# Kernel optimization log

Measured on AMD Instinct MI355X. Metric: run time of the kernel, lower is better.

The kernel has to match this reference:

```python
import jax, jax.numpy as jnp
import numpy as np

B, C, T = 128, 9, 2048
R = T // 4            # reduced_timesteps after two MaxPool1d(2)
N = B * R             # total graph nodes
E_SINGLE = 8192       # edges per sample graph (avg degree 16 over R nodes)
HID = 128
OUT = 12


def setup_inputs():
    key = jax.random.key(0)
    ks = jax.random.split(key, 14)
    x = jax.random.normal(ks[0], (B, C, T), jnp.float32)
    # per-sample graph, replicated with offset i*R per batch element (as in forward)
    single = jax.random.randint(ks[1], (2, E_SINGLE), 0, R)
    offsets = (jnp.arange(B) * R)[None, :, None]
    edge_index = (single[:, None, :] + offsets).reshape(2, -1)  # [2, B*E_SINGLE]

    def lin(k, fan_in, shape):
        return jax.random.normal(k, shape, jnp.float32) / np.sqrt(fan_in)

    return {
        "x": x,
        "edge_index": edge_index,
        "conv1_w": lin(ks[2], C * 5, (16, C, 5)),
        "conv1_b": jnp.zeros((16,), jnp.float32),
        "conv2_w": lin(ks[3], 16 * 5, (32, 16, 5)),
        "conv2_b": jnp.zeros((32,), jnp.float32),
        "gcn1_w": lin(ks[4], 32, (32, HID)),
        "gcn1_b": jnp.zeros((HID,), jnp.float32),
        "gcn2_w": lin(ks[5], HID, (HID, HID)),
        "gcn2_b": jnp.zeros((HID,), jnp.float32),
        "fc_w": lin(ks[6], HID, (HID, OUT)),
        "fc_b": jnp.zeros((OUT,), jnp.float32),
    }


def _gcn_conv(h, edge_index, w, b, n):
    # PyG GCNConv: linear -> add self-loops -> sym-normalized sum aggregation -> + bias
    h = h @ w
    loops = jnp.arange(n)
    row = jnp.concatenate([edge_index[0], loops])  # source
    col = jnp.concatenate([edge_index[1], loops])  # target (aggregation)
    deg = jax.ops.segment_sum(jnp.ones(col.shape, h.dtype), col, num_segments=n)
    dis = jnp.where(deg > 0, jax.lax.rsqrt(jnp.maximum(deg, 1e-12)), 0.0)
    norm = dis[row] * dis[col]                      # [E+N]
    out = jax.ops.segment_sum(norm[:, None] * h[row], col, num_segments=n)
    return out + b


def _temporal_conv(x, w1, b1, w2, b2):
    dn = ("NCH", "OIH", "NCH")
    h = jax.lax.conv_general_dilated(x, w1, (1,), [(2, 2)], dimension_numbers=dn)
    h = jax.nn.relu(h + b1[None, :, None])
    h = jax.lax.reduce_window(h, -jnp.inf, jax.lax.max, (1, 1, 2), (1, 1, 2), "VALID")
    h = jax.lax.conv_general_dilated(h, w2, (1,), [(2, 2)], dimension_numbers=dn)
    h = jax.nn.relu(h + b2[None, :, None])
    h = jax.lax.reduce_window(h, -jnp.inf, jax.lax.max, (1, 1, 2), (1, 1, 2), "VALID")
    return h  # [B, 32, R]


def reference(x, edge_index, conv1_w, conv1_b, conv2_w, conv2_b,
              gcn1_w, gcn1_b, gcn2_w, gcn2_b, fc_w, fc_b):
    h = _temporal_conv(x, conv1_w, conv1_b, conv2_w, conv2_b)   # [B, 32, R]
    nodes = h.transpose(0, 2, 1).reshape(B * R, 32)             # [N, 32]
    g = jax.nn.relu(_gcn_conv(nodes, edge_index, gcn1_w, gcn1_b, N))
    g = jax.nn.relu(_gcn_conv(g, edge_index, gcn2_w, gcn2_b, N))
    g = g.reshape(B, R, HID).mean(axis=1)                       # [B, HID]
    return g @ fc_w + fc_b                                      # [B, OUT]
```

## Files before the change

kernel.cpp:

```cpp
#include <hip/hip_runtime.h>
#include <hip/hip_bf16.h>

#define BB   128
#define CIN  9
#define TT   2048
#define RR   512
#define NN   (BB*RR)
#define HID  128
#define NOUT 12

typedef __attribute__((ext_vector_type(8))) short short8;
typedef __attribute__((ext_vector_type(4))) float f32x4;

static __device__ inline unsigned short f2bf(float f) {
    unsigned int u = __float_as_uint(f);
    unsigned int r = (u + 0x7fffu + ((u >> 16) & 1u)) >> 16;
    return (unsigned short)r;
}
static __device__ inline float bf2f(unsigned short u) {
    return __uint_as_float(((unsigned int)u) << 16);
}

__global__ __launch_bounds__(256) void k_prep(const int* __restrict__ ei, int E, int es,
        float* __restrict__ Af32, float* __restrict__ dis,
        const float* __restrict__ g2w, unsigned short* __restrict__ w2t) {
    int tid = threadIdx.x;
    if (blockIdx.x == 0) {
        __shared__ int cnt[512];
        cnt[tid] = 0; cnt[tid + 256] = 0;
        __syncthreads();
        for (int i = tid; i < es; i += 256) atomicAdd(&cnt[ei[E + i]], 1);
        __syncthreads();
        dis[tid]       = rsqrtf((float)cnt[tid] + 1.0f);
        dis[tid + 256] = rsqrtf((float)cnt[tid + 256] + 1.0f);
        for (int idx = tid; idx < 128 * 128; idx += 256) {
            int c2 = idx >> 7, f = idx & 127;
            w2t[f * 128 + c2] = f2bf(g2w[idx]);
        }
    } else {
        float4* dst = (float4*)(Af32 + (size_t)(blockIdx.x - 1) * 2048);
        float4 z = make_float4(0.f, 0.f, 0.f, 0.f);
        dst[tid] = z;
        dst[tid + 256] = z;
    }
}

__global__ __launch_bounds__(256) void k_scatter(const int* __restrict__ ei, int E, int es,
        const float* __restrict__ dis, float* __restrict__ Af32) {
    int i = blockIdx.x * 256 + threadIdx.x;
    if (i < es) {
        int row = ei[i], col = ei[E + i];
        atomicAdd(&Af32[col * 512 + row], dis[row] * dis[col]);
    } else if (i < es + 512) {
        int r = i - es;
        float d = dis[r];
        atomicAdd(&Af32[r * 512 + r], d * d);
    }
}

__global__ __launch_bounds__(512) void k_convs(const float* __restrict__ x,
        const float* __restrict__ w1, const float* __restrict__ b1,
        const float* __restrict__ w2, const float* __restrict__ b2,
        unsigned short* __restrict__ nodesT,
        const float* __restrict__ Af32, unsigned short* __restrict__ Ab16) {
    __shared__ float sx[CIN][268];
    __shared__ float s1[16][132];
    int tid = threadIdx.x;

    if (blockIdx.x >= 1024) {
        int idx0 = (((blockIdx.x - 1024) << 9) + tid) << 3;
        float4 v0 = *(const float4*)&Af32[idx0];
        float4 v1 = *(const float4*)&Af32[idx0 + 4];
        ushort4 o0, o1;
        o0.x = f2bf(v0.x); o0.y = f2bf(v0.y); o0.z = f2bf(v0.z); o0.w = f2bf(v0.w);
        o1.x = f2bf(v1.x); o1.y = f2bf(v1.y); o1.z = f2bf(v1.z); o1.w = f2bf(v1.w);
        *(ushort4*)&Ab16[idx0] = o0;
        *(ushort4*)&Ab16[idx0 + 4] = o1;
        return;
    }

    int cb = blockIdx.x;
    int b  = cb >> 3;
    int r0 = (cb & 7) * 64;
    int wv   = __builtin_amdgcn_readfirstlane(tid >> 6);
    int lane = tid & 63;

    for (int idx = tid; idx < CIN * 268; idx += 512) {
        int c = idx / 268, j = idx - c * 268;
        int g = 4 * r0 - 6 + j;
        float v = 0.f;
        if (g >= 0 && g < TT) v = x[(b * CIN + c) * TT + g];
        sx[c][j] = v;
    }
    __syncthreads();

    {
        int c1a = wv * 2, c1b = wv * 2 + 1;
        float biasA = b1[c1a], biasB = b1[c1b];
        for (int pp = lane; pp < 132; pp += 64) {
            int p = 2 * r0 - 2 + pp;
            float valA = 0.f, valB = 0.f;
            if (p >= 0 && p < 1024) {
                float a0A = biasA, a1A = biasA, a0B = biasB, a1B = biasB;
#pragma unroll
                for (int c = 0; c < CIN; ++c) {
                    const float2* px = (const float2*)&sx[c][2 * pp];
                    float2 q0 = px[0], q1 = px[1], q2 = px[2];
                    {
                        const float* wp = &w1[(c1a * CIN + c) * 5];
                        float k0 = wp[0], k1 = wp[1], k2 = wp[2], k3 = wp[3], k4 = wp[4];
                        a0A += q0.x*k0 + q0.y*k1 + q1.x*k2 + q1.y*k3 + q2.x*k4;
                        a1A += q0.y*k0 + q1.x*k1 + q1.y*k2 + q2.x*k3 + q2.y*k4;
                    }
                    {
                        const float* wp = &w1[(c1b * CIN + c) * 5];
                        float k0 = wp[0], k1 = wp[1], k2 = wp[2], k3 = wp[3], k4 = wp[4];
                        a0B += q0.x*k0 + q0.y*k1 + q1.x*k2 + q1.y*k3 + q2.x*k4;
                        a1B += q0.y*k0 + q1.x*k1 + q1.y*k2 + q2.x*k3 + q2.y*k4;
                    }
                }
                valA = fmaxf(fmaxf(a0A, a1A), 0.f);
                valB = fmaxf(fmaxf(a0B, a1B), 0.f);
            }
            s1[c1a][pp] = valA;
            s1[c1b][pp] = valB;
        }
    }
    __syncthreads();

    int rl = lane;
    float acc0[4], acc1[4];
#pragma unroll
    for (int o = 0; o < 4; ++o) {
        float bv = b2[wv * 4 + o];
        acc0[o] = bv; acc1[o] = bv;
    }
#pragma unroll
    for (int c = 0; c < 16; ++c) {
        const float2* ps = (const float2*)&s1[c][2 * rl];
        float2 q0 = ps[0], q1 = ps[1], q2 = ps[2];
#pragma unroll
        for (int o = 0; o < 4; ++o) {
            const float* wp = &w2[((wv * 4 + o) * 16 + c) * 5];
            float k0 = wp[0], k1 = wp[1], k2 = wp[2], k3 = wp[3], k4 = wp[4];
            acc0[o] += q0.x*k0 + q0.y*k1 + q1.x*k2 + q1.y*k3 + q2.x*k4;
            acc1[o] += q0.y*k0 + q1.x*k1 + q1.y*k2 + q2.x*k3 + q2.y*k4;
        }
    }
    int n = r0 + rl;
    unsigned short* np = nodesT + ((size_t)b * 32 + wv * 4) * 512 + n;
    np[0]    = f2bf(fmaxf(fmaxf(acc0[0], acc1[0]), 0.f));
    np[512]  = f2bf(fmaxf(fmaxf(acc0[1], acc1[1]), 0.f));
    np[1024] = f2bf(fmaxf(fmaxf(acc0[2], acc1[2]), 0.f));
    np[1536] = f2bf(fmaxf(fmaxf(acc0[3], acc1[3]), 0.f));
}

__global__ __launch_bounds__(256) void k_agg1(const unsigned short* __restrict__ Ab,
        const unsigned short* __restrict__ nT, const float* __restrict__ w1,
        const float* __restrict__ b1, unsigned short* __restrict__ h16) {
    __shared__ unsigned short sA[128][72];
    __shared__ unsigned short sN[32][72];
    __shared__ float sAgg[128][33];
    __shared__ float sw1[32 * 128];
    int tid = threadIdx.x;
    int b  = blockIdx.x >> 2;
    int rb = blockIdx.x & 3;
    int r0 = rb * 128;
    const unsigned short* nb = nT + (size_t)b * 32 * 512;

    {
        const float4* src = (const float4*)w1;
        float4* dst = (float4*)sw1;
#pragma unroll
        for (int i = 0; i < 4; ++i) dst[tid + i * 256] = src[tid + i * 256];
    }

    int wv = tid >> 6, lane = tid & 63;
    int l15 = lane & 15, quad = lane >> 4;
    int mB = wv * 32;
    f32x4 acc[2][2];
#pragma unroll
    for (int i = 0; i < 2; ++i)
#pragma unroll
        for (int j = 0; j < 2; ++j) acc[i][j] = (f32x4){0.f, 0.f, 0.f, 0.f};

    for (int kt = 0; kt < 8; ++kt) {
        int k0 = kt * 64;
        __syncthreads();
#pragma unroll
        for (int i = 0; i < 8; ++i) {
            int idx = tid + i * 256;
            int row = idx >> 4, c4 = (idx & 15) * 4;
            *(ushort4*)&sA[row][c4] = *(const ushort4*)&Ab[(size_t)(r0 + row) * 512 + k0 + c4];
        }
#pragma unroll
        for (int i = 0; i < 2; ++i) {
            int idx = tid + i * 256;
            int f = idx >> 4, c4 = (idx & 15) * 4;
            *(ushort4*)&sN[f][c4] = *(const ushort4*)&nb[(size_t)f * 512 + k0 + c4];
        }
        __syncthreads();
#pragma unroll
        for (int ks = 0; ks < 2; ++ks) {
            int kk = ks * 32 + quad * 8;
            short8 av0 = *(const short8*)&sA[mB + l15][kk];
            short8 av1 = *(const short8*)&sA[mB + 16 + l15][kk];
            short8 bv0 = *(const short8*)&sN[l15][kk];
            short8 bv1 = *(const short8*)&sN[16 + l15][kk];
            acc[0][0] = __builtin_amdgcn_mfma_f32_16x16x32_bf16(av0, bv0, acc[0][0], 0, 0, 0);
            acc[0][1] = __builtin_amdgcn_mfma_f32_16x16x32_bf16(av0, bv1, acc[0][1], 0, 0, 0);
            acc[1][0] = __builtin_amdgcn_mfma_f32_16x16x32_bf16(av1, bv0, acc[1][0], 0, 0, 0);
            acc[1][1] = __builtin_amdgcn_mfma_f32_16x16x32_bf16(av1, bv1, acc[1][1], 0, 0, 0);
        }
    }
    __syncthreads();
#pragma unroll
    for (int mi = 0; mi < 2; ++mi)
#pragma unroll
        for (int ni = 0; ni < 2; ++ni)
#pragma unroll
            for (int r = 0; r < 4; ++r)
                sAgg[mB + mi * 16 + quad * 4 + r][ni * 16 + l15] = acc[mi][ni][r];
    __syncthreads();

    int fq = tid & 31;
    int ng = tid >> 5;
    float4 bv = *(const float4*)&b1[fq * 4];
    for (int ch = 0; ch < 4; ++ch) {
        float a[4][4];
#pragma unroll
        for (int j = 0; j < 4; ++j)
#pragma unroll
            for (int q = 0; q < 4; ++q) a[j][q] = 0.f;
#pragma unroll
        for (int c = 0; c < 32; ++c) {
            float4 wvv = *(const float4*)&sw1[c * 128 + fq * 4];
#pragma unroll
            for (int j = 0; j < 4; ++j) {
                float xc = sAgg[ch * 32 + ng * 4 + j][c];
                a[j][0] += xc * wvv.x; a[j][1] += xc * wvv.y;
                a[j][2] += xc * wvv.z; a[j][3] += xc * wvv.w;
            }
        }
#pragma unroll
        for (int j = 0; j < 4; ++j) {
            ushort4 o;
            o.x = f2bf(fmaxf(a[j][0] + bv.x, 0.f));
            o.y = f2bf(fmaxf(a[j][1] + bv.y, 0.f));
            o.z = f2bf(fmaxf(a[j][2] + bv.z, 0.f));
            o.w = f2bf(fmaxf(a[j][3] + bv.w, 0.f));
            *(ushort4*)&h16[(size_t)(b * 512 + r0 + ch * 32 + ng * 4 + j) * 128 + fq * 4] = o;
        }
    }
}

__global__ __launch_bounds__(256) void k_lin2(const unsigned short* __restrict__ g16,
        const unsigned short* __restrict__ w2t, unsigned short* __restrict__ tT) {
    __shared__ __align__(16) unsigned short smem2[64 * 136 + 128 * 136];
    unsigned short (*srow)[136] = (unsigned short (*)[136])smem2;
    unsigned short (*swT)[136]  = (unsigned short (*)[136])&smem2[64 * 136];
    unsigned short (*sOut)[72]  = (unsigned short (*)[72])smem2;
    int tid = threadIdx.x;
    int nbase = blockIdx.x * 64;

    {
        const ushort4* src = (const ushort4*)(g16 + (size_t)nbase * 128);
#pragma unroll
        for (int i = 0; i < 8; ++i) {
            int idx = tid + i * 256;
            int row = idx >> 5, col4 = idx & 31;
            ushort4 v = src[idx];
            *(ushort4*)&srow[row][col4 * 4] = v;
        }
    }
    {
        const ushort4* src = (const ushort4*)w2t;
#pragma unroll
        for (int i = 0; i < 16; ++i) {
            int idx = tid + i * 256;
            int f = idx >> 5, c4 = idx & 31;
            ushort4 v = src[idx];
            *(ushort4*)&swT[f][c4 * 4] = v;
        }
    }
    __syncthreads();

    int wv  = tid >> 6;
    int lane = tid & 63;
    int m0 = wv * 16;
    int l15 = lane & 15;
    int quad = lane >> 4;
    f32x4 acc[8];
#pragma unroll
    for (int nt = 0; nt < 8; ++nt) acc[nt] = (f32x4){0.f, 0.f, 0.f, 0.f};
#pragma unroll
    for (int kc = 0; kc < 4; ++kc) {
        int k0 = kc * 32 + quad * 8;
        short8 a = *(const short8*)&srow[m0 + l15][k0];
#pragma unroll
        for (int nt = 0; nt < 8; ++nt) {
            short8 b = *(const short8*)&swT[nt * 16 + l15][k0];
            acc[nt] = __builtin_amdgcn_mfma_f32_16x16x32_bf16(a, b, acc[nt], 0, 0, 0);
        }
    }
    __syncthreads();

#pragma unroll
    for (int nt = 0; nt < 8; ++nt) {
        ushort4 o;
        o.x = f2bf(acc[nt][0]); o.y = f2bf(acc[nt][1]);
        o.z = f2bf(acc[nt][2]); o.w = f2bf(acc[nt][3]);
        *(ushort4*)&sOut[nt * 16 + l15][m0 + quad * 4] = o;
    }
    __syncthreads();

    int b = nbase >> 9;
    int rl0 = nbase & 511;
#pragma unroll
    for (int i = 0; i < 8; ++i) {
        int idx = tid + i * 256;
        int col = idx >> 4, r4 = (idx & 15) * 4;
        ushort4 v = *(ushort4*)&sOut[col][r4];
        *(ushort4*)&tT[((size_t)(b * 128 + col)) * 512 + rl0 + r4] = v;
    }
}

__global__ __launch_bounds__(256) void k_agg2(const unsigned short* __restrict__ Ab,
        const unsigned short* __restrict__ tT, const float* __restrict__ b2,
        float* __restrict__ partial) {
    __shared__ unsigned short sA[128][72];
    __shared__ unsigned short sB[128][72];
    __shared__ float sred[2][128];
    int tid = threadIdx.x;
    int b  = blockIdx.x >> 2;
    int rb = blockIdx.x & 3;
    int r0 = rb * 128;
    const unsigned short* tb = tT + (size_t)b * 128 * 512;
    int wv = tid >> 6, lane = tid & 63;
    int l15 = lane & 15, quad = lane >> 4;
    int wr = wv >> 1, wc = wv & 1;
    f32x4 acc[4][4];
#pragma unroll
    for (int i = 0; i < 4; ++i)
#pragma unroll
        for (int j = 0; j < 4; ++j) acc[i][j] = (f32x4){0.f, 0.f, 0.f, 0.f};

    for (int kt = 0; kt < 8; ++kt) {
        int k0 = kt * 64;
        __syncthreads();
#pragma unroll
        for (int i = 0; i < 8; ++i) {
            int idx = tid + i * 256;
            int row = idx >> 4, c4 = (idx & 15) * 4;
            *(ushort4*)&sA[row][c4] = *(const ushort4*)&Ab[(size_t)(r0 + row) * 512 + k0 + c4];
        }
#pragma unroll
        for (int i = 0; i < 8; ++i) {
            int idx = tid + i * 256;
            int row = idx >> 4, c4 = (idx & 15) * 4;
            *(ushort4*)&sB[row][c4] = *(const ushort4*)&tb[(size_t)row * 512 + k0 + c4];
        }
        __syncthreads();
#pragma unroll
        for (int ks = 0; ks < 2; ++ks) {
            int kk = ks * 32 + quad * 8;
            short8 av[4], bfr[4];
#pragma unroll
            for (int mi = 0; mi < 4; ++mi)
                av[mi] = *(const short8*)&sA[wr * 64 + mi * 16 + l15][kk];
#pragma unroll
            for (int ni = 0; ni < 4; ++ni)
                bfr[ni] = *(const short8*)&sB[wc * 64 + ni * 16 + l15][kk];
#pragma unroll
            for (int mi = 0; mi < 4; ++mi)
#pragma unroll
                for (int ni = 0; ni < 4; ++ni)
                    acc[mi][ni] = __builtin_amdgcn_mfma_f32_16x16x32_bf16(av[mi], bfr[ni], acc[mi][ni], 0, 0, 0);
        }
    }

#pragma unroll
    for (int ni = 0; ni < 4; ++ni) {
        int col = wc * 64 + ni * 16 + l15;
        float bc = b2[col];
        float s = 0.f;
#pragma unroll
        for (int mi = 0; mi < 4; ++mi)
#pragma unroll
            for (int r = 0; r < 4; ++r)
                s += fmaxf(acc[mi][ni][r] + bc, 0.f);
        s += __shfl_xor(s, 16);
        s += __shfl_xor(s, 32);
        if (quad == 0) sred[wr][col] = s;
    }
    __syncthreads();
    if (tid < 128)
        partial[(size_t)blockIdx.x * 128 + tid] = sred[0][tid] + sred[1][tid];
}

__global__ __launch_bounds__(128) void k_fc(const float* __restrict__ partial,
        const float* __restrict__ fw, const float* __restrict__ fb,
        float* __restrict__ out) {
    __shared__ float sm[HID];
    int b = blockIdx.x, f = threadIdx.x;
    float acc = 0.f;
#pragma unroll
    for (int j = 0; j < 4; ++j) acc += partial[(size_t)(b * 4 + j) * 128 + f];
    sm[f] = acc * (1.0f / RR);
    __syncthreads();
    if (f < NOUT) {
        float s = fb[f];
#pragma unroll
        for (int c = 0; c < HID; ++c) s += sm[c] * fw[c * NOUT + f];
        out[b * NOUT + f] = s;
    }
}

extern "C" void kernel_launch(void* const* d_in, const int* in_sizes, int n_in,
                              void* d_out, int out_size, void* d_ws, size_t ws_size,
                              hipStream_t stream) {
    const float* x   = (const float*)d_in[0];
    const int*   ei  = (const int*)d_in[1];
    const float* c1w = (const float*)d_in[2];
    const float* c1b = (const float*)d_in[3];
    const float* c2w = (const float*)d_in[4];
    const float* c2b = (const float*)d_in[5];
    const float* g1w = (const float*)d_in[6];
    const float* g1b = (const float*)d_in[7];
    const float* g2w = (const float*)d_in[8];
    const float* g2b = (const float*)d_in[9];
    const float* fw  = (const float*)d_in[10];
    const float* fb  = (const float*)d_in[11];
    float* out = (float*)d_out;
    int E  = in_sizes[1] / 2;
    int es = E / BB;

    char* ws = (char*)d_ws;
    unsigned short* nodesT = (unsigned short*)(ws);
    unsigned short* h1     = (unsigned short*)(ws + (4u << 20));
    unsigned short* tT     = (unsigned short*)(ws + (20u << 20));
    float* Af32            = (float*)(ws + (36u << 20));
    unsigned short* Ab16   = (unsigned short*)(ws + (37u << 20));
    float* partial         = (float*)(ws + (37u << 20) + (512u << 10));
    float* dis             = (float*)(ws + (37u << 20) + (768u << 10));
    unsigned short* w2t    = (unsigned short*)(ws + (37u << 20) + (772u << 10));

    k_prep<<<129, 256, 0, stream>>>(ei, E, es, Af32, dis, g2w, w2t);
    k_scatter<<<(es + 512 + 255) / 256, 256, 0, stream>>>(ei, E, es, dis, Af32);

    k_convs<<<1024 + 64, 512, 0, stream>>>(x, c1w, c1b, c2w, c2b, nodesT, Af32, Ab16);

    k_agg1<<<512, 256, 0, stream>>>(Ab16, nodesT, g1w, g1b, h1);

    k_lin2<<<NN / 64, 256, 0, stream>>>(h1, w2t, tT);
    k_agg2<<<512, 256, 0, stream>>>(Ab16, tT, g2b, partial);

    k_fc<<<BB, 128, 0, stream>>>(partial, fw, fb, out);
}
```

Before: 187.9 us.

## Fold adjacency build into a dedicated block of the conv kernel

Result: slower. 249.8 us (+32.9%).

```diff
diff --git a/kernel.cpp b/kernel.cpp
--- a/kernel.cpp
+++ b/kernel.cpp
@@ -21,65 +21,56 @@
     return __uint_as_float(((unsigned int)u) << 16);
 }
 
-__global__ __launch_bounds__(256) void k_prep(const int* __restrict__ ei, int E, int es,
-        float* __restrict__ Af32, float* __restrict__ dis,
-        const float* __restrict__ g2w, unsigned short* __restrict__ w2t) {
-    int tid = threadIdx.x;
-    if (blockIdx.x == 0) {
-        __shared__ int cnt[512];
-        cnt[tid] = 0; cnt[tid + 256] = 0;
-        __syncthreads();
-        for (int i = tid; i < es; i += 256) atomicAdd(&cnt[ei[E + i]], 1);
-        __syncthreads();
-        dis[tid]       = rsqrtf((float)cnt[tid] + 1.0f);
-        dis[tid + 256] = rsqrtf((float)cnt[tid + 256] + 1.0f);
-        for (int idx = tid; idx < 128 * 128; idx += 256) {
-            int c2 = idx >> 7, f = idx & 127;
-            w2t[f * 128 + c2] = f2bf(g2w[idx]);
-        }
-    } else {
-        float4* dst = (float4*)(Af32 + (size_t)(blockIdx.x - 1) * 2048);
-        float4 z = make_float4(0.f, 0.f, 0.f, 0.f);
-        dst[tid] = z;
-        dst[tid + 256] = z;
-    }
-}
-
-__global__ __launch_bounds__(256) void k_scatter(const int* __restrict__ ei, int E, int es,
-        const float* __restrict__ dis, float* __restrict__ Af32) {
-    int i = blockIdx.x * 256 + threadIdx.x;
-    if (i < es) {
-        int row = ei[i], col = ei[E + i];
-        atomicAdd(&Af32[col * 512 + row], dis[row] * dis[col]);
-    } else if (i < es + 512) {
-        int r = i - es;
-        float d = dis[r];
-        atomicAdd(&Af32[r * 512 + r], d * d);
-    }
-}
-
-__global__ __launch_bounds__(512) void k_convs(const float* __restrict__ x,
+__global__ __launch_bounds__(512, 4) void k_convs(const float* __restrict__ x,
         const float* __restrict__ w1, const float* __restrict__ b1,
         const float* __restrict__ w2, const float* __restrict__ b2,
         unsigned short* __restrict__ nodesT,
-        const float* __restrict__ Af32, unsigned short* __restrict__ Ab16) {
+        const int* __restrict__ ei, int E, int es,
+        float* __restrict__ Af32, unsigned short* __restrict__ Ab16,
+        const float* __restrict__ g2w, unsigned short* __restrict__ w2t) {
     __shared__ float sx[CIN][268];
     __shared__ float s1[16][132];
     int tid = threadIdx.x;
 
-    if (blockIdx.x >= 1024) {
-        int idx0 = (((blockIdx.x - 1024) << 9) + tid) << 3;
-        float4 v0 = *(const float4*)&Af32[idx0];
-        float4 v1 = *(const float4*)&Af32[idx0 + 4];
-        ushort4 o0, o1;
-        o0.x = f2bf(v0.x); o0.y = f2bf(v0.y); o0.z = f2bf(v0.z); o0.w = f2bf(v0.w);
-        o1.x = f2bf(v1.x); o1.y = f2bf(v1.y); o1.z = f2bf(v1.z); o1.w = f2bf(v1.w);
-        *(ushort4*)&Ab16[idx0] = o0;
-        *(ushort4*)&Ab16[idx0 + 4] = o1;
+    if (blockIdx.x == 0) {
+        __shared__ int   cnt[512];
+        __shared__ float sdis[512];
+        float4 z = make_float4(0.f, 0.f, 0.f, 0.f);
+        float4* az = (float4*)Af32;
+#pragma unroll
+        for (int i = 0; i < 128; ++i) az[tid + i * 512] = z;
+        cnt[tid] = 0;
+        __syncthreads();
+        for (int i = tid; i < es; i += 512) atomicAdd(&cnt[ei[E + i]], 1);
+        __syncthreads();
+        float d = rsqrtf((float)cnt[tid] + 1.0f);
+        sdis[tid] = d;
+        __syncthreads();
+        for (int i = tid; i < es; i += 512) {
+            int row = ei[i], col = ei[E + i];
+            atomicAdd(&Af32[col * 512 + row], sdis[row] * sdis[col]);
+        }
+        atomicAdd(&Af32[tid * 512 + tid], d * d);
+        __syncthreads();
+        __threadfence();
+        for (int i = tid; i < 512 * 512 / 8; i += 512) {
+            int idx0 = i << 3;
+            float4 v0 = *(const float4*)&Af32[idx0];
+            float4 v1 = *(const float4*)&Af32[idx0 + 4];
+            ushort4 o0, o1;
+            o0.x = f2bf(v0.x); o0.y = f2bf(v0.y); o0.z = f2bf(v0.z); o0.w = f2bf(v0.w);
+            o1.x = f2bf(v1.x); o1.y = f2bf(v1.y); o1.z = f2bf(v1.z); o1.w = f2bf(v1.w);
+            *(ushort4*)&Ab16[idx0] = o0;
+            *(ushort4*)&Ab16[idx0 + 4] = o1;
+        }
+        for (int idx = tid; idx < 128 * 128; idx += 512) {
+            int c2 = idx >> 7, f = idx & 127;
+            w2t[f * 128 + c2] = f2bf(g2w[idx]);
+        }
         return;
     }
 
-    int cb = blockIdx.x;
+    int cb = blockIdx.x - 1;
     int b  = cb >> 3;
     int r0 = (cb & 7) * 64;
     int wv   = __builtin_amdgcn_readfirstlane(tid >> 6);
@@ -97,6 +88,14 @@
     {
         int c1a = wv * 2, c1b = wv * 2 + 1;
         float biasA = b1[c1a], biasB = b1[c1b];
+        float wA[CIN][5], wB[CIN][5];
+#pragma unroll
+        for (int c = 0; c < CIN; ++c)
+#pragma unroll
+            for (int k = 0; k < 5; ++k) {
+                wA[c][k] = w1[(c1a * CIN + c) * 5 + k];
+                wB[c][k] = w1[(c1b * CIN + c) * 5 + k];
+            }
         for (int pp = lane; pp < 132; pp += 64) {
             int p = 2 * r0 - 2 + pp;
             float valA = 0.f, valB = 0.f;
@@ -106,18 +105,10 @@
                 for (int c = 0; c < CIN; ++c) {
                     const float2* px = (const float2*)&sx[c][2 * pp];
                     float2 q0 = px[0], q1 = px[1], q2 = px[2];
-                    {
-                        const float* wp = &w1[(c1a * CIN + c) * 5];
-                        float k0 = wp[0], k1 = wp[1], k2 = wp[2], k3 = wp[3], k4 = wp[4];
-                        a0A += q0.x*k0 + q0.y*k1 + q1.x*k2 + q1.y*k3 + q2.x*k4;
-                        a1A += q0.y*k0 + q1.x*k1 + q1.y*k2 + q2.x*k3 + q2.y*k4;
-                    }
-                    {
-                        const float* wp = &w1[(c1b * CIN + c) * 5];
-                        float k0 = wp[0], k1 = wp[1], k2 = wp[2], k3 = wp[3], k4 = wp[4];
-                        a0B += q0.x*k0 + q0.y*k1 + q1.x*k2 + q1.y*k3 + q2.x*k4;
-                        a1B += q0.y*k0 + q1.x*k1 + q1.y*k2 + q2.x*k3 + q2.y*k4;
-                    }
+                    a0A += q0.x*wA[c][0] + q0.y*wA[c][1] + q1.x*wA[c][2] + q1.y*wA[c][3] + q2.x*wA[c][4];
+                    a1A += q0.y*wA[c][0] + q1.x*wA[c][1] + q1.y*wA[c][2] + q2.x*wA[c][3] + q2.y*wA[c][4];
+                    a0B += q0.x*wB[c][0] + q0.y*wB[c][1] + q1.x*wB[c][2] + q1.y*wB[c][3] + q2.x*wB[c][4];
+                    a1B += q0.y*wB[c][0] + q1.x*wB[c][1] + q1.y*wB[c][2] + q2.x*wB[c][3] + q2.y*wB[c][4];
                 }
                 valA = fmaxf(fmaxf(a0A, a1A), 0.f);
                 valB = fmaxf(fmaxf(a0B, a1B), 0.f);
@@ -442,13 +433,10 @@
     float* Af32            = (float*)(ws + (36u << 20));
     unsigned short* Ab16   = (unsigned short*)(ws + (37u << 20));
     float* partial         = (float*)(ws + (37u << 20) + (512u << 10));
-    float* dis             = (float*)(ws + (37u << 20) + (768u << 10));
     unsigned short* w2t    = (unsigned short*)(ws + (37u << 20) + (772u << 10));
 
-    k_prep<<<129, 256, 0, stream>>>(ei, E, es, Af32, dis, g2w, w2t);
-    k_scatter<<<(es + 512 + 255) / 256, 256, 0, stream>>>(ei, E, es, dis, Af32);
-
-    k_convs<<<1024 + 64, 512, 0, stream>>>(x, c1w, c1b, c2w, c2b, nodesT, Af32, Ab16);
+    k_convs<<<1025, 512, 0, stream>>>(x, c1w, c1b, c2w, c2b, nodesT,
+                                      ei, E, es, Af32, Ab16, g2w, w2t);
 
     k_agg1<<<512, 256, 0, stream>>>(Ab16, nodesT, g1w, g1b, h1);
 
```
